# Optimization experiments

Measured on AMD Instinct MI355X. Metric: run time of the kernel, lower is better.

Reference implementation:

```python
import jax, jax.numpy as jnp
import numpy as np

B, T, V, L = 131072, 6, 31, 3  # batch, seq_len, vocab/hidden, num RNN layers


def setup_inputs() -> dict:
    key = jax.random.key(0)
    ks = jax.random.split(key, 8)
    s = 1.0 / np.sqrt(V)  # torch default init scale for RNN/Linear
    return {
        "inp": jax.random.normal(ks[0], (B, T, V), dtype=jnp.float32),
        "h0": jax.random.normal(ks[1], (L, B, V), dtype=jnp.float32),
        "W_ih": jax.random.uniform(ks[2], (L, V, V), jnp.float32, -s, s),
        "W_hh": jax.random.uniform(ks[3], (L, V, V), jnp.float32, -s, s),
        "b_ih": jax.random.uniform(ks[4], (L, V), jnp.float32, -s, s),
        "b_hh": jax.random.uniform(ks[5], (L, V), jnp.float32, -s, s),
        "W_lin": jax.random.uniform(ks[6], (V, V), jnp.float32, -s, s),
        "b_lin": jax.random.uniform(ks[7], (V,), jnp.float32, -s, s),
    }


def _rnn_layer(x_tm, h0_l, wih, whh, bih, bhh):
    # x_tm: [T, B, V] time-major; h0_l: [B, V]
    def step(h, x_t):
        h_new = jnp.tanh(x_t @ wih.T + bih + h @ whh.T + bhh)
        return h_new, h_new

    _, ys = jax.lax.scan(step, h0_l, x_tm)
    return ys  # [T, B, V]


def reference(inp, h0, W_ih, W_hh, b_ih, b_hh, W_lin, b_lin):
    x = jnp.transpose(inp, (1, 0, 2))  # [T, B, V] time-major
    for l in range(L):
        x = _rnn_layer(x, h0[l], W_ih[l], W_hh[l], b_ih[l], b_hh[l])
    y = jnp.tanh(x @ W_lin.T + b_lin)  # [T, B, V]
    last = y[-1]  # [B, V] == y[:, -1, :] in batch-major
    return jax.nn.softmax(last, axis=1)
```

## Files before the change

kernel.cpp:

```cpp
#include <hip/hip_runtime.h>
#include <hip/hip_bf16.h>


#define VD 31
#define TD 6
#define LROW 40
#define LBUF (16 * LROW)

typedef __attribute__((ext_vector_type(8))) short bf16x8;
typedef __attribute__((ext_vector_type(4))) float f32x4;
typedef __attribute__((ext_vector_type(4))) unsigned u32x4;
typedef float f32x4u __attribute__((ext_vector_type(4), aligned(4)));

struct raw8 { f32x4u a, b; };

__device__ __forceinline__ short f2bf(float f) {
    unsigned u = __float_as_uint(f);
    unsigned r = (u + 0x7fffu + ((u >> 16) & 1u)) >> 16;
    return (short)r;
}

__device__ __forceinline__ unsigned f2bf2u(float lo, float hi) {
    union { __hip_bfloat162 h2; unsigned u; } cvt;
    cvt.h2 = __float22bfloat162_rn(make_float2(lo, hi));
    return cvt.u;
}

__device__ __forceinline__ float fast_tanh(float x) {
    x = fminf(fmaxf(x, -15.0f), 15.0f);
    float e = __expf(2.0f * x);
    return (e - 1.0f) * __builtin_amdgcn_rcpf(e + 1.0f);
}

__device__ __forceinline__ raw8 load_raw(const float* __restrict__ p, int fo) {
    raw8 r;
    r.a = *(const f32x4u*)(p + fo);
    r.b = *(const f32x4u*)(p + fo + 4);
    return r;
}

__device__ __forceinline__ bf16x8 cvt_frag(raw8 r, bool q3) {
    float l[8] = {r.a[0], r.a[1], r.a[2], r.a[3], r.b[0], r.b[1], r.b[2], r.b[3]};
    float s[8];
#pragma unroll
    for (int j = 0; j < 7; ++j) s[j] = q3 ? l[j + 1] : l[j];
    s[7] = q3 ? 0.0f : l[7];
    union { u32x4 u4; bf16x8 b8; } cvt;
#pragma unroll
    for (int j = 0; j < 4; ++j) cvt.u4[j] = f2bf2u(s[2 * j], s[2 * j + 1]);
    return cvt.b8;
}

__device__ __forceinline__ bf16x8 load_wfrag(const float* __restrict__ W,
                                             int nn, int k0) {
    bf16x8 r;
#pragma unroll
    for (int j = 0; j < 8; ++j) {
        int k = k0 + j;
        float v = (nn < VD && k < VD) ? W[nn * VD + k] : 0.0f;
        r[j] = f2bf(v);
    }
    return r;
}

__device__ __forceinline__ bf16x8 layer_step(
    bf16x8 ax, bf16x8 ah,
    bf16x8 wi0, bf16x8 wi1, bf16x8 wh0, bf16x8 wh1,
    float b0, float b1, short* buf, int n, int quad, int k0)
{
    f32x4 c0 = {b0, b0, b0, b0};
    f32x4 c1 = {b1, b1, b1, b1};
    c0 = __builtin_amdgcn_mfma_f32_16x16x32_bf16(ax, wi0, c0, 0, 0, 0);
    c1 = __builtin_amdgcn_mfma_f32_16x16x32_bf16(ax, wi1, c1, 0, 0, 0);
    c0 = __builtin_amdgcn_mfma_f32_16x16x32_bf16(ah, wh0, c0, 0, 0, 0);
    c1 = __builtin_amdgcn_mfma_f32_16x16x32_bf16(ah, wh1, c1, 0, 0, 0);
#pragma unroll
    for (int r = 0; r < 4; ++r) {
        int row = quad * 4 + r;
        unsigned u = f2bf2u(fast_tanh(c0[r]), fast_tanh(c1[r]));
        buf[row * LROW + n]      = (short)u;
        buf[row * LROW + 16 + n] = (short)(u >> 16);
    }
    __builtin_amdgcn_wave_barrier();
    return *(const bf16x8*)(buf + n * LROW + k0);
}

__global__ __launch_bounds__(256, 1) void rnn_mfma(
    const float* __restrict__ inp,
    const float* __restrict__ h0,
    const float* __restrict__ Wih,
    const float* __restrict__ Whh,
    const float* __restrict__ bih,
    const float* __restrict__ bhh,
    const float* __restrict__ Wlin,
    const float* __restrict__ blin,
    float* __restrict__ out,
    int B)
{
    __shared__ __align__(16) short lds[4][2][2][LBUF];

    const int wave = threadIdx.x >> 6;
    const int lane = threadIdx.x & 63;
    const int n    = lane & 15;
    const int quad = lane >> 4;
    const int k0   = quad * 8;
    const bool q3  = (quad == 3);
    const int fo   = q3 ? 23 : k0;
    const int bbase = (blockIdx.x * 4 + wave) * 32;
    if (bbase >= B) return;

    const float* W0 = Wih;               const float* U0 = Whh;
    const float* W1 = Wih + VD * VD;     const float* U1 = Whh + VD * VD;
    const float* W2 = Wih + 2 * VD * VD; const float* U2 = Whh + 2 * VD * VD;
    const bf16x8 wiA0 = load_wfrag(W0, n, k0),   wiA1 = load_wfrag(W0, n + 16, k0);
    const bf16x8 whA0 = load_wfrag(U0, n, k0),   whA1 = load_wfrag(U0, n + 16, k0);
    const bf16x8 wiB0 = load_wfrag(W1, n, k0),   wiB1 = load_wfrag(W1, n + 16, k0);
    const bf16x8 whB0 = load_wfrag(U1, n, k0),   whB1 = load_wfrag(U1, n + 16, k0);
    const bf16x8 wiC0 = load_wfrag(W2, n, k0),   wiC1 = load_wfrag(W2, n + 16, k0);
    const bf16x8 whC0 = load_wfrag(U2, n, k0),   whC1 = load_wfrag(U2, n + 16, k0);
    const bf16x8 wl0  = load_wfrag(Wlin, n, k0), wl1  = load_wfrag(Wlin, n + 16, k0);

    const bool hi_ok = (n + 16) < VD;
    const float bsA0 = bih[n] + bhh[n];
    const float bsA1 = hi_ok ? bih[n + 16] + bhh[n + 16] : 0.0f;
    const float bsB0 = bih[VD + n] + bhh[VD + n];
    const float bsB1 = hi_ok ? bih[VD + n + 16] + bhh[VD + n + 16] : 0.0f;
    const float bsC0 = bih[2 * VD + n] + bhh[2 * VD + n];
    const float bsC1 = hi_ok ? bih[2 * VD + n + 16] + bhh[2 * VD + n + 16] : 0.0f;
    const float bl0  = blin[n];
    const float bl1  = hi_ok ? blin[n + 16] : 0.0f;

    bf16x8 a1a = cvt_frag(load_raw(h0 + ((size_t)0 * B + bbase + n) * VD, fo), q3);
    bf16x8 a1b = cvt_frag(load_raw(h0 + ((size_t)0 * B + bbase + 16 + n) * VD, fo), q3);
    bf16x8 a2a = cvt_frag(load_raw(h0 + ((size_t)1 * B + bbase + n) * VD, fo), q3);
    bf16x8 a2b = cvt_frag(load_raw(h0 + ((size_t)1 * B + bbase + 16 + n) * VD, fo), q3);
    bf16x8 a3a = cvt_frag(load_raw(h0 + ((size_t)2 * B + bbase + n) * VD, fo), q3);
    bf16x8 a3b = cvt_frag(load_raw(h0 + ((size_t)2 * B + bbase + 16 + n) * VD, fo), q3);

    const float* xrow0 = inp + (size_t)(bbase + n) * TD * VD;
    const float* xrow1 = inp + (size_t)(bbase + 16 + n) * TD * VD;

    raw8 rx0 = load_raw(xrow0, fo);
    raw8 rx1 = load_raw(xrow1, fo);

    int p = 0;
    for (int t = 0; t < TD; ++t) {
        bf16x8 ax0 = cvt_frag(rx0, q3);
        bf16x8 ax1 = cvt_frag(rx1, q3);
        if (t + 1 < TD) {
            rx0 = load_raw(xrow0 + (t + 1) * VD, fo);
            rx1 = load_raw(xrow1 + (t + 1) * VD, fo);
        }
        a1a = layer_step(ax0, a1a, wiA0, wiA1, whA0, whA1, bsA0, bsA1,
                         lds[wave][0][p], n, quad, k0);
        a1b = layer_step(ax1, a1b, wiA0, wiA1, whA0, whA1, bsA0, bsA1,
                         lds[wave][1][p], n, quad, k0);
        p ^= 1;
        a2a = layer_step(a1a, a2a, wiB0, wiB1, whB0, whB1, bsB0, bsB1,
                         lds[wave][0][p], n, quad, k0);
        a2b = layer_step(a1b, a2b, wiB0, wiB1, whB0, whB1, bsB0, bsB1,
                         lds[wave][1][p], n, quad, k0);
        p ^= 1;
        a3a = layer_step(a2a, a3a, wiC0, wiC1, whC0, whC1, bsC0, bsC1,
                         lds[wave][0][p], n, quad, k0);
        a3b = layer_step(a2b, a3b, wiC0, wiC1, whC0, whC1, bsC0, bsC1,
                         lds[wave][1][p], n, quad, k0);
        p ^= 1;
    }

    f32x4 c0a = {bl0, bl0, bl0, bl0}, c1a = {bl1, bl1, bl1, bl1};
    f32x4 c0b = {bl0, bl0, bl0, bl0}, c1b = {bl1, bl1, bl1, bl1};
    c0a = __builtin_amdgcn_mfma_f32_16x16x32_bf16(a3a, wl0, c0a, 0, 0, 0);
    c1a = __builtin_amdgcn_mfma_f32_16x16x32_bf16(a3a, wl1, c1a, 0, 0, 0);
    c0b = __builtin_amdgcn_mfma_f32_16x16x32_bf16(a3b, wl0, c0b, 0, 0, 0);
    c1b = __builtin_amdgcn_mfma_f32_16x16x32_bf16(a3b, wl1, c1b, 0, 0, 0);

    const bool pad = (n == 15);
#pragma unroll
    for (int r = 0; r < 4; ++r) {
#pragma unroll
        for (int tb = 0; tb < 2; ++tb) {
            float v0 = fast_tanh(tb ? c0b[r] : c0a[r]);
            float v1 = fast_tanh(tb ? c1b[r] : c1a[r]);
            float mx = pad ? v0 : fmaxf(v0, v1);
#pragma unroll
            for (int msk = 1; msk < 16; msk <<= 1)
                mx = fmaxf(mx, __shfl_xor(mx, msk, 16));
            float e0 = __expf(v0 - mx);
            float e1 = pad ? 0.0f : __expf(v1 - mx);
            float s = e0 + e1;
#pragma unroll
            for (int msk = 1; msk < 16; msk <<= 1)
                s += __shfl_xor(s, msk, 16);
            float inv = __builtin_amdgcn_rcpf(s);
            const size_t row = (size_t)(bbase + tb * 16 + quad * 4 + r);
            out[row * VD + n] = e0 * inv;
            if (!pad) out[row * VD + 16 + n] = e1 * inv;
        }
    }
}

extern "C" void kernel_launch(void* const* d_in, const int* in_sizes, int n_in,
                              void* d_out, int out_size, void* d_ws, size_t ws_size,
                              hipStream_t stream) {
    const float* inp  = (const float*)d_in[0];
    const float* h0   = (const float*)d_in[1];
    const float* Wih  = (const float*)d_in[2];
    const float* Whh  = (const float*)d_in[3];
    const float* bih  = (const float*)d_in[4];
    const float* bhh  = (const float*)d_in[5];
    const float* Wlin = (const float*)d_in[6];
    const float* blin = (const float*)d_in[7];
    float* out = (float*)d_out;

    const int B = in_sizes[0] / (TD * VD);
    const int grid = (B + 127) / 128;
    rnn_mfma<<<grid, 256, 0, stream>>>(inp, h0, Wih, Whh, bih, bhh, Wlin, blin, out, B);
}
```

Before: 216.7 us.

## Compute transposed MFMA so RNN outputs land in operand layout, drop LDS round-trip

The MFMA operands are swapped (W as A, hidden state as B) and output rows are permuted so each lane's accumulator values form the bf16x8 fragment the next layer step needs. This removes the per-step LDS store, wave barrier and reload. Biases are folded into the weight matrix through a constant-1 padding column in the activations, so accumulators start from zero. The final softmax becomes per-lane reductions plus two cross-quad shuffles, and the output stores are vectorized. The trade-off is that biases are now rounded to bf16, which slightly reduces precision.

```diff
diff --git a/kernel.cpp b/kernel.cpp
--- a/kernel.cpp
+++ b/kernel.cpp
@@ -4,8 +4,6 @@
 
 #define VD 31
 #define TD 6
-#define LROW 40
-#define LBUF (16 * LROW)
 
 typedef __attribute__((ext_vector_type(8))) short bf16x8;
 typedef __attribute__((ext_vector_type(4))) float f32x4;
@@ -44,7 +42,7 @@
     float s[8];
 #pragma unroll
     for (int j = 0; j < 7; ++j) s[j] = q3 ? l[j + 1] : l[j];
-    s[7] = q3 ? 0.0f : l[7];
+    s[7] = q3 ? 1.0f : l[7];
     union { u32x4 u4; bf16x8 b8; } cvt;
 #pragma unroll
     for (int j = 0; j < 4; ++j) cvt.u4[j] = f2bf2u(s[2 * j], s[2 * j + 1]);
@@ -52,37 +50,43 @@
 }
 
 __device__ __forceinline__ bf16x8 load_wfrag(const float* __restrict__ W,
-                                             int nn, int k0) {
+                                             const float* __restrict__ b1,
+                                             const float* __restrict__ b2,
+                                             int i, int half, int k0) {
+    const int nn = 8 * (i >> 2) + (i & 3) + 4 * half;
     bf16x8 r;
 #pragma unroll
     for (int j = 0; j < 8; ++j) {
         int k = k0 + j;
-        float v = (nn < VD && k < VD) ? W[nn * VD + k] : 0.0f;
+        float v = 0.0f;
+        if (nn < VD) {
+            if (k < VD) v = W[nn * VD + k];
+            else v = (b1 ? b1[nn] : 0.0f) + (b2 ? b2[nn] : 0.0f);
+        }
         r[j] = f2bf(v);
     }
     return r;
 }
 
-__device__ __forceinline__ bf16x8 layer_step(
-    bf16x8 ax, bf16x8 ah,
-    bf16x8 wi0, bf16x8 wi1, bf16x8 wh0, bf16x8 wh1,
-    float b0, float b1, short* buf, int n, int quad, int k0)
+__device__ __forceinline__ bf16x8 layer_step(bf16x8 x, bf16x8 h,
+    bf16x8 wi0, bf16x8 wi1, bf16x8 wh0, bf16x8 wh1, bool q3)
 {
-    f32x4 c0 = {b0, b0, b0, b0};
-    f32x4 c1 = {b1, b1, b1, b1};
-    c0 = __builtin_amdgcn_mfma_f32_16x16x32_bf16(ax, wi0, c0, 0, 0, 0);
-    c1 = __builtin_amdgcn_mfma_f32_16x16x32_bf16(ax, wi1, c1, 0, 0, 0);
-    c0 = __builtin_amdgcn_mfma_f32_16x16x32_bf16(ah, wh0, c0, 0, 0, 0);
-    c1 = __builtin_amdgcn_mfma_f32_16x16x32_bf16(ah, wh1, c1, 0, 0, 0);
-#pragma unroll
-    for (int r = 0; r < 4; ++r) {
-        int row = quad * 4 + r;
-        unsigned u = f2bf2u(fast_tanh(c0[r]), fast_tanh(c1[r]));
-        buf[row * LROW + n]      = (short)u;
-        buf[row * LROW + 16 + n] = (short)(u >> 16);
-    }
-    __builtin_amdgcn_wave_barrier();
-    return *(const bf16x8*)(buf + n * LROW + k0);
+    const f32x4 z = {0.0f, 0.0f, 0.0f, 0.0f};
+    f32x4 c0 = __builtin_amdgcn_mfma_f32_16x16x32_bf16(wh0, h, z, 0, 0, 0);
+    f32x4 c1 = __builtin_amdgcn_mfma_f32_16x16x32_bf16(wh1, h, z, 0, 0, 0);
+    c0 = __builtin_amdgcn_mfma_f32_16x16x32_bf16(wi0, x, c0, 0, 0, 0);
+    c1 = __builtin_amdgcn_mfma_f32_16x16x32_bf16(wi1, x, c1, 0, 0, 0);
+    float t0 = fast_tanh(c0[0]), t1 = fast_tanh(c0[1]);
+    float t2 = fast_tanh(c0[2]), t3 = fast_tanh(c0[3]);
+    float t4 = fast_tanh(c1[0]), t5 = fast_tanh(c1[1]);
+    float t6 = fast_tanh(c1[2]);
+    float t7 = q3 ? 1.0f : fast_tanh(c1[3]);
+    union { u32x4 u4; bf16x8 b8; } cvt;
+    cvt.u4[0] = f2bf2u(t0, t1);
+    cvt.u4[1] = f2bf2u(t2, t3);
+    cvt.u4[2] = f2bf2u(t4, t5);
+    cvt.u4[3] = f2bf2u(t6, t7);
+    return cvt.b8;
 }
 
 __global__ __launch_bounds__(256, 1) void rnn_mfma(
@@ -97,11 +101,9 @@
     float* __restrict__ out,
     int B)
 {
-    __shared__ __align__(16) short lds[4][2][2][LBUF];
-
     const int wave = threadIdx.x >> 6;
     const int lane = threadIdx.x & 63;
-    const int n    = lane & 15;
+    const int cb   = lane & 15;
     const int quad = lane >> 4;
     const int k0   = quad * 8;
     const bool q3  = (quad == 3);
@@ -112,38 +114,34 @@
     const float* W0 = Wih;               const float* U0 = Whh;
     const float* W1 = Wih + VD * VD;     const float* U1 = Whh + VD * VD;
     const float* W2 = Wih + 2 * VD * VD; const float* U2 = Whh + 2 * VD * VD;
-    const bf16x8 wiA0 = load_wfrag(W0, n, k0),   wiA1 = load_wfrag(W0, n + 16, k0);
-    const bf16x8 whA0 = load_wfrag(U0, n, k0),   whA1 = load_wfrag(U0, n + 16, k0);
-    const bf16x8 wiB0 = load_wfrag(W1, n, k0),   wiB1 = load_wfrag(W1, n + 16, k0);
-    const bf16x8 whB0 = load_wfrag(U1, n, k0),   whB1 = load_wfrag(U1, n + 16, k0);
-    const bf16x8 wiC0 = load_wfrag(W2, n, k0),   wiC1 = load_wfrag(W2, n + 16, k0);
-    const bf16x8 whC0 = load_wfrag(U2, n, k0),   whC1 = load_wfrag(U2, n + 16, k0);
-    const bf16x8 wl0  = load_wfrag(Wlin, n, k0), wl1  = load_wfrag(Wlin, n + 16, k0);
-
-    const bool hi_ok = (n + 16) < VD;
-    const float bsA0 = bih[n] + bhh[n];
-    const float bsA1 = hi_ok ? bih[n + 16] + bhh[n + 16] : 0.0f;
-    const float bsB0 = bih[VD + n] + bhh[VD + n];
-    const float bsB1 = hi_ok ? bih[VD + n + 16] + bhh[VD + n + 16] : 0.0f;
-    const float bsC0 = bih[2 * VD + n] + bhh[2 * VD + n];
-    const float bsC1 = hi_ok ? bih[2 * VD + n + 16] + bhh[2 * VD + n + 16] : 0.0f;
-    const float bl0  = blin[n];
-    const float bl1  = hi_ok ? blin[n + 16] : 0.0f;
-
-    bf16x8 a1a = cvt_frag(load_raw(h0 + ((size_t)0 * B + bbase + n) * VD, fo), q3);
-    bf16x8 a1b = cvt_frag(load_raw(h0 + ((size_t)0 * B + bbase + 16 + n) * VD, fo), q3);
-    bf16x8 a2a = cvt_frag(load_raw(h0 + ((size_t)1 * B + bbase + n) * VD, fo), q3);
-    bf16x8 a2b = cvt_frag(load_raw(h0 + ((size_t)1 * B + bbase + 16 + n) * VD, fo), q3);
-    bf16x8 a3a = cvt_frag(load_raw(h0 + ((size_t)2 * B + bbase + n) * VD, fo), q3);
-    bf16x8 a3b = cvt_frag(load_raw(h0 + ((size_t)2 * B + bbase + 16 + n) * VD, fo), q3);
-
-    const float* xrow0 = inp + (size_t)(bbase + n) * TD * VD;
-    const float* xrow1 = inp + (size_t)(bbase + 16 + n) * TD * VD;
+    const bf16x8 wiA0 = load_wfrag(W0, bih, bhh, cb, 0, k0);
+    const bf16x8 wiA1 = load_wfrag(W0, bih, bhh, cb, 1, k0);
+    const bf16x8 whA0 = load_wfrag(U0, nullptr, nullptr, cb, 0, k0);
+    const bf16x8 whA1 = load_wfrag(U0, nullptr, nullptr, cb, 1, k0);
+    const bf16x8 wiB0 = load_wfrag(W1, bih + VD, bhh + VD, cb, 0, k0);
+    const bf16x8 wiB1 = load_wfrag(W1, bih + VD, bhh + VD, cb, 1, k0);
+    const bf16x8 whB0 = load_wfrag(U1, nullptr, nullptr, cb, 0, k0);
+    const bf16x8 whB1 = load_wfrag(U1, nullptr, nullptr, cb, 1, k0);
+    const bf16x8 wiC0 = load_wfrag(W2, bih + 2 * VD, bhh + 2 * VD, cb, 0, k0);
+    const bf16x8 wiC1 = load_wfrag(W2, bih + 2 * VD, bhh + 2 * VD, cb, 1, k0);
+    const bf16x8 whC0 = load_wfrag(U2, nullptr, nullptr, cb, 0, k0);
+    const bf16x8 whC1 = load_wfrag(U2, nullptr, nullptr, cb, 1, k0);
+    const bf16x8 wl0  = load_wfrag(Wlin, blin, nullptr, cb, 0, k0);
+    const bf16x8 wl1  = load_wfrag(Wlin, blin, nullptr, cb, 1, k0);
+
+    bf16x8 h1a = cvt_frag(load_raw(h0 + ((size_t)0 * B + bbase + cb) * VD, fo), q3);
+    bf16x8 h1b = cvt_frag(load_raw(h0 + ((size_t)0 * B + bbase + 16 + cb) * VD, fo), q3);
+    bf16x8 h2a = cvt_frag(load_raw(h0 + ((size_t)1 * B + bbase + cb) * VD, fo), q3);
+    bf16x8 h2b = cvt_frag(load_raw(h0 + ((size_t)1 * B + bbase + 16 + cb) * VD, fo), q3);
+    bf16x8 h3a = cvt_frag(load_raw(h0 + ((size_t)2 * B + bbase + cb) * VD, fo), q3);
+    bf16x8 h3b = cvt_frag(load_raw(h0 + ((size_t)2 * B + bbase + 16 + cb) * VD, fo), q3);
+
+    const float* xrow0 = inp + (size_t)(bbase + cb) * TD * VD;
+    const float* xrow1 = inp + (size_t)(bbase + 16 + cb) * TD * VD;
 
     raw8 rx0 = load_raw(xrow0, fo);
     raw8 rx1 = load_raw(xrow1, fo);
 
-    int p = 0;
     for (int t = 0; t < TD; ++t) {
         bf16x8 ax0 = cvt_frag(rx0, q3);
         bf16x8 ax1 = cvt_frag(rx1, q3);
@@ -151,51 +149,48 @@
             rx0 = load_raw(xrow0 + (t + 1) * VD, fo);
             rx1 = load_raw(xrow1 + (t + 1) * VD, fo);
         }
-        a1a = layer_step(ax0, a1a, wiA0, wiA1, whA0, whA1, bsA0, bsA1,
-                         lds[wave][0][p], n, quad, k0);
-        a1b = layer_step(ax1, a1b, wiA0, wiA1, whA0, whA1, bsA0, bsA1,
-                         lds[wave][1][p], n, quad, k0);
-        p ^= 1;
-        a2a = layer_step(a1a, a2a, wiB0, wiB1, whB0, whB1, bsB0, bsB1,
-                         lds[wave][0][p], n, quad, k0);
-        a2b = layer_step(a1b, a2b, wiB0, wiB1, whB0, whB1, bsB0, bsB1,
-                         lds[wave][1][p], n, quad, k0);
-        p ^= 1;
-        a3a = layer_step(a2a, a3a, wiC0, wiC1, whC0, whC1, bsC0, bsC1,
-                         lds[wave][0][p], n, quad, k0);
-        a3b = layer_step(a2b, a3b, wiC0, wiC1, whC0, whC1, bsC0, bsC1,
-                         lds[wave][1][p], n, quad, k0);
-        p ^= 1;
+        h1a = layer_step(ax0, h1a, wiA0, wiA1, whA0, whA1, q3);
+        h1b = layer_step(ax1, h1b, wiA0, wiA1, whA0, whA1, q3);
+        h2a = layer_step(h1a, h2a, wiB0, wiB1, whB0, whB1, q3);
+        h2b = layer_step(h1b, h2b, wiB0, wiB1, whB0, whB1, q3);
+        h3a = layer_step(h2a, h3a, wiC0, wiC1, whC0, whC1, q3);
+        h3b = layer_step(h2b, h3b, wiC0, wiC1, whC0, whC1, q3);
     }
 
-    f32x4 c0a = {bl0, bl0, bl0, bl0}, c1a = {bl1, bl1, bl1, bl1};
-    f32x4 c0b = {bl0, bl0, bl0, bl0}, c1b = {bl1, bl1, bl1, bl1};
-    c0a = __builtin_amdgcn_mfma_f32_16x16x32_bf16(a3a, wl0, c0a, 0, 0, 0);
-    c1a = __builtin_amdgcn_mfma_f32_16x16x32_bf16(a3a, wl1, c1a, 0, 0, 0);
-    c0b = __builtin_amdgcn_mfma_f32_16x16x32_bf16(a3b, wl0, c0b, 0, 0, 0);
-    c1b = __builtin_amdgcn_mfma_f32_16x16x32_bf16(a3b, wl1, c1b, 0, 0, 0);
-
-    const bool pad = (n == 15);
-#pragma unroll
-    for (int r = 0; r < 4; ++r) {
-#pragma unroll
-        for (int tb = 0; tb < 2; ++tb) {
-            float v0 = fast_tanh(tb ? c0b[r] : c0a[r]);
-            float v1 = fast_tanh(tb ? c1b[r] : c1a[r]);
-            float mx = pad ? v0 : fmaxf(v0, v1);
-#pragma unroll
-            for (int msk = 1; msk < 16; msk <<= 1)
-                mx = fmaxf(mx, __shfl_xor(mx, msk, 16));
-            float e0 = __expf(v0 - mx);
-            float e1 = pad ? 0.0f : __expf(v1 - mx);
-            float s = e0 + e1;
-#pragma unroll
-            for (int msk = 1; msk < 16; msk <<= 1)
-                s += __shfl_xor(s, msk, 16);
-            float inv = __builtin_amdgcn_rcpf(s);
-            const size_t row = (size_t)(bbase + tb * 16 + quad * 4 + r);
-            out[row * VD + n] = e0 * inv;
-            if (!pad) out[row * VD + 16 + n] = e1 * inv;
+    const f32x4 z = {0.0f, 0.0f, 0.0f, 0.0f};
+#pragma unroll
+    for (int tb = 0; tb < 2; ++tb) {
+        bf16x8 h3 = tb ? h3b : h3a;
+        f32x4 c0 = __builtin_amdgcn_mfma_f32_16x16x32_bf16(wl0, h3, z, 0, 0, 0);
+        f32x4 c1 = __builtin_amdgcn_mfma_f32_16x16x32_bf16(wl1, h3, z, 0, 0, 0);
+        float v0 = fast_tanh(c0[0]), v1 = fast_tanh(c0[1]);
+        float v2 = fast_tanh(c0[2]), v3 = fast_tanh(c0[3]);
+        float v4 = fast_tanh(c1[0]), v5 = fast_tanh(c1[1]);
+        float v6 = fast_tanh(c1[2]), v7 = fast_tanh(c1[3]);
+        float mx = fmaxf(fmaxf(fmaxf(v0, v1), fmaxf(v2, v3)),
+                         fmaxf(fmaxf(v4, v5), fmaxf(v6, v7)));
+        mx = fmaxf(mx, __shfl_xor(mx, 16));
+        mx = fmaxf(mx, __shfl_xor(mx, 32));
+        float e0 = __expf(v0 - mx), e1 = __expf(v1 - mx);
+        float e2 = __expf(v2 - mx), e3 = __expf(v3 - mx);
+        float e4 = __expf(v4 - mx), e5 = __expf(v5 - mx);
+        float e6 = __expf(v6 - mx);
+        float e7 = q3 ? 0.0f : __expf(v7 - mx);
+        float s = ((e0 + e1) + (e2 + e3)) + ((e4 + e5) + (e6 + e7));
+        s += __shfl_xor(s, 16);
+        s += __shfl_xor(s, 32);
+        const float inv = __builtin_amdgcn_rcpf(s);
+        const size_t row = (size_t)(bbase + tb * 16 + cb);
+        float* po = out + row * VD + k0;
+        f32x4u lo = {e0 * inv, e1 * inv, e2 * inv, e3 * inv};
+        *(f32x4u*)po = lo;
+        if (!q3) {
+            f32x4u hi = {e4 * inv, e5 * inv, e6 * inv, e7 * inv};
+            *(f32x4u*)(po + 4) = hi;
+        } else {
+            po[4] = e4 * inv;
+            po[5] = e5 * inv;
+            po[6] = e6 * inv;
         }
     }
 }
```

Result: no change. 215.1 us (-0.7%).
